# Kernel tuning notes

Measured on AMD Instinct MI355X. Metric: run time of the kernel, lower is better.

The kernel has to match this reference:

```python
import jax, jax.numpy as jnp
import numpy as np

B, S, D, H, FF, L, U = 64, 256, 128, 8, 512, 4, 5000
N, E, FEA, HW, CED, TD = 40000, 160000, 32, 16, 16, 6
DH = D // H


def _ln(x, g, b):
    m = jnp.mean(x, -1, keepdims=True)
    v = jnp.var(x, -1, keepdims=True)
    return (x - m) * jax.lax.rsqrt(v + 1e-5) * g + b


def _sin_pe(s, d):
    pos = jnp.arange(s, dtype=jnp.float32)[:, None]
    div = jnp.exp(jnp.arange(0, d, 2, dtype=jnp.float32) * (-np.log(10000.0) / d))
    ang = pos * div  # [S, D/2]
    return jnp.stack([jnp.sin(ang), jnp.cos(ang)], -1).reshape(s, d)


def setup_inputs() -> dict:
    key = jax.random.key(0)
    ks = jax.random.split(key, 40)
    sc = 0.02
    inp = {}
    inp['node_feature'] = jax.random.normal(ks[0], (N, FEA), jnp.float32)
    inp['edge_index'] = jax.random.randint(ks[1], (2, E), 0, N)
    inp['traj_x'] = jax.random.randint(ks[2], (B, S), 0, N)
    inp['temporal_x'] = jax.random.normal(ks[3], (B, S, TD), jnp.float32)
    inp['user_id_x'] = jax.random.randint(ks[4], (B, 1), 0, U)
    inp['mask'] = jnp.ones((B, S), jnp.int32)
    inp['end_idx'] = jax.random.randint(ks[5], (B,), 0, S)
    inp['idx_without_end'] = jax.random.randint(ks[6], (B,), 0, S)
    inp['temporal_mat_x'] = jax.random.uniform(ks[7], (B, S, S), jnp.float32) * 3600.0
    inp['dis_mat_x'] = jax.random.uniform(ks[8], (B, S, S), jnp.float32) * 5000.0
    inp['highway_x'] = jax.random.randint(ks[9], (B, S), 0, HW)
    inp['lambda2'] = jnp.float32(0.5)
    # --- learned parameters ---
    inp['gnn_w1'] = jax.random.normal(ks[10], (FEA, D), jnp.float32) * sc
    inp['gnn_b1'] = jnp.zeros((D,), jnp.float32)
    inp['gnn_w2'] = jax.random.normal(ks[11], (D, D), jnp.float32) * sc
    inp['gnn_b2'] = jnp.zeros((D,), jnp.float32)
    inp['ue_tab'] = jax.random.normal(ks[12], (U, D), jnp.float32) * sc
    inp['ce_tab'] = jax.random.normal(ks[13], (HW, CED), jnp.float32) * sc
    inp['fl_w'] = jax.random.normal(ks[14], (TD + CED, D), jnp.float32) * sc
    inp['fl_b'] = jnp.zeros((D,), jnp.float32)
    inp['wqkv'] = jax.random.normal(ks[15], (L, D, 3 * D), jnp.float32) * sc
    inp['bqkv'] = jnp.zeros((L, 3 * D), jnp.float32)
    inp['wo'] = jax.random.normal(ks[16], (L, D, D), jnp.float32) * sc
    inp['bo'] = jnp.zeros((L, D), jnp.float32)
    inp['ln1_g'] = jnp.ones((L, D), jnp.float32)
    inp['ln1_b'] = jnp.zeros((L, D), jnp.float32)
    inp['ln2_g'] = jnp.ones((L, D), jnp.float32)
    inp['ln2_b'] = jnp.zeros((L, D), jnp.float32)
    inp['ffn_w1'] = jax.random.normal(ks[17], (L, D, FF), jnp.float32) * sc
    inp['ffn_b1'] = jnp.zeros((L, FF), jnp.float32)
    inp['ffn_w2'] = jax.random.normal(ks[18], (L, FF, D), jnp.float32) * sc
    inp['ffn_b2'] = jnp.zeros((L, D), jnp.float32)
    inp['head_w'] = jax.random.normal(ks[19], (D, U), jnp.float32) * sc
    inp['head_b'] = jnp.zeros((U,), jnp.float32)
    return inp


def reference(node_feature, edge_index, traj_x, temporal_x, user_id_x, mask,
              end_idx, idx_without_end, temporal_mat_x, dis_mat_x, highway_x,
              lambda2,
              gnn_w1, gnn_b1, gnn_w2, gnn_b2, ue_tab, ce_tab, fl_w, fl_b,
              wqkv, bqkv, wo, bo, ln1_g, ln1_b, ln2_g, ln2_b,
              ffn_w1, ffn_b1, ffn_w2, ffn_b2, head_w, head_b):
    # --- spatial (road-network) GNN encoder: spe ---
    src, dst = edge_index[0], edge_index[1]
    deg = jax.ops.segment_sum(jnp.ones((E,), jnp.float32), dst, num_segments=N)
    h = node_feature
    for W, b in ((gnn_w1, gnn_b1), (gnn_w2, gnn_b2)):
        agg = jax.ops.segment_sum(h[src], dst, num_segments=N) / (deg[:, None] + 1.0)
        h = jax.nn.relu((h + agg) @ W + b)
    spe = h  # [N, D]
    # --- embedding fusion ---
    ce = ce_tab[highway_x]                                  # [B,S,CED]
    ue = ue_tab[user_id_x]                                  # [B,1,D] broadcast
    fuse = jax.nn.relu(jnp.concatenate([temporal_x, ce], -1) @ fl_w + fl_b)
    x = spe[traj_x] + ue + fuse                             # [B,S,D]
    x = x + _sin_pe(S, D)[None]
    # --- relative temporal/distance attention bias ---
    rel = lambda2 * jnp.log1p(temporal_mat_x) + (1.0 - lambda2) * jnp.log1p(dis_mat_x)
    mbias = jnp.where(mask[:, None, None, :] > 0, 0.0, -1e9)
    bias = mbias - rel[:, None]                             # [B,1,S,S]
    scale = 1.0 / float(np.sqrt(DH))
    for l in range(L):
        qkv = x @ wqkv[l] + bqkv[l]
        q, k, v = jnp.split(qkv, 3, axis=-1)
        q = q.reshape(B, S, H, DH).transpose(0, 2, 1, 3)
        k = k.reshape(B, S, H, DH).transpose(0, 2, 1, 3)
        v = v.reshape(B, S, H, DH).transpose(0, 2, 1, 3)
        scores = jnp.einsum('bhqd,bhkd->bhqk', q, k) * scale + bias
        a = jax.nn.softmax(scores, -1)
        o = jnp.einsum('bhqk,bhkd->bhqd', a, v).transpose(0, 2, 1, 3).reshape(B, S, D)
        x = _ln(x + o @ wo[l] + bo[l], ln1_g[l], ln1_b[l])
        f = jax.nn.relu(x @ ffn_w1[l] + ffn_b1[l]) @ ffn_w2[l] + ffn_b2[l]
        x = _ln(x + f, ln2_g[l], ln2_b[l])
    # --- gather last token + classifier head ---
    traj_emb = x[jnp.arange(B), end_idx]                    # [B,D]
    return traj_emb @ head_w + head_b                       # [B,U]
```

## Files before the change

### kernel.cpp

```cpp
#include <hip/hip_runtime.h>
#include <hip/hip_fp16.h>
#include <cstdint>
#include <cstddef>

typedef unsigned short u16;
typedef __attribute__((ext_vector_type(8))) short short8;
typedef __attribute__((ext_vector_type(4))) float f32x4;

#define B_   64
#define S_   256
#define D_   128
#define H_   8
#define DH_  16
#define FF_  512
#define L_   4
#define U_   5000
#define UP_  5120
#define N_   40000
#define NP_  40064
#define E_   160000
#define FEA_ 32
#define HWY_ 16
#define CED_ 16
#define TD_  6
#define NSCB 157
#define UB_CNT_END 160
#define UB_CVT_END 1592
#define UB_TOTAL   5688

static __device__ __forceinline__ u16 f2b(float f) {
    unsigned int u = __float_as_uint(f);
    unsigned int r = (u + 0x7FFFu + ((u >> 16) & 1u)) >> 16;
    return (u16)r;
}
static __device__ __forceinline__ float b2f(u16 u) {
    return __uint_as_float(((unsigned int)u) << 16);
}
static __device__ __forceinline__ u16 f2h(float f) {
    return __half_as_ushort(__float2half(f));
}
static __device__ __forceinline__ float h2f(u16 u) {
    return __half2float(__ushort_as_half(u));
}

static __device__ __forceinline__ void gload16(const void* g, void* l) {
    __builtin_amdgcn_global_load_lds(
        (const __attribute__((address_space(1))) unsigned int*)g,
        (__attribute__((address_space(3))) unsigned int*)l,
        16, 0, 0);
}

struct UberArgs {
    const float* csrc[7];
    u16* cdst[7];
    int K[7], Npad[7], Nsrc[7], Kp[7], base[7];
    const float* tm; const float* dm; const int* maskp; const float* lambda2;
    u16* bias; int* cnt;
};

__global__ __launch_bounds__(256) void k_uber(UberArgs a) {
    __shared__ float tile[32][33];
    int bid = blockIdx.x, tid = threadIdx.x;
    if (bid < UB_CNT_END) {
        int idx = bid * 256 + tid;
        if (idx < NP_) a.cnt[idx] = 0;
        return;
    }
    if (bid < UB_CVT_END) {
        int t = 0;
#pragma unroll
        for (int i = 1; i < 7; ++i) t += (bid >= a.base[i]);
        int rb = bid - a.base[t];
        int K = a.K[t], Npad = a.Npad[t], Nsrc = a.Nsrc[t], Kp = a.Kp[t];
        int nbn = Npad >> 5, nbk = Kp >> 5;
        int per = nbn * nbk;
        int l = rb / per, rem = rb - l * per;
        int n0 = (rem % nbn) * 32, k0 = (rem / nbn) * 32;
        const float* in = a.csrc[t];
        u16* outp = a.cdst[t];
        int j = tid & 31, i2 = tid >> 5;
#pragma unroll
        for (int r = 0; r < 4; ++r) {
            int k = k0 + i2 + r * 8, n = n0 + j;
            tile[i2 + r * 8][j] = (k < K && n < Nsrc) ? in[(size_t)l * K * Nsrc + (size_t)k * Nsrc + n] : 0.f;
        }
        __syncthreads();
#pragma unroll
        for (int r = 0; r < 4; ++r) {
            int n = n0 + i2 + r * 8, k = k0 + j;
            if (n < Npad && k < Kp)
                outp[(size_t)l * Npad * Kp + (size_t)n * Kp + k] = f2b(tile[j][i2 + r * 8]);
        }
        return;
    }
    int t4 = (bid - UB_CVT_END) * 256 + tid;
    const int total = B_ * S_ * S_ / 4;
    if (t4 >= total) return;
// ... 19 lines not shown
__global__ __launch_bounds__(256) void k_scanA(const int* __restrict__ cnt, int* __restrict__ part) {
    __shared__ int sh[256];
    int idx = blockIdx.x * 256 + threadIdx.x;
    sh[threadIdx.x] = (idx < NP_) ? cnt[idx] : 0;
    __syncthreads();
    for (int o = 128; o > 0; o >>= 1) {
        if (threadIdx.x < o) sh[threadIdx.x] += sh[threadIdx.x + o];
        __syncthreads();
    }
    if (threadIdx.x == 0) part[blockIdx.x] = sh[0];
}

__global__ __launch_bounds__(256) void k_scanB(const int* __restrict__ cnt, const int* __restrict__ part,
                                               int* __restrict__ off, int* __restrict__ cursor) {
    __shared__ int sh[256];
    __shared__ int bsum;
    int tid = threadIdx.x;
    int pv = (tid < blockIdx.x) ? part[tid] : 0;
    sh[tid] = pv;
    __syncthreads();
    for (int o = 128; o > 0; o >>= 1) {
        if (tid < o) sh[tid] += sh[tid + o];
        __syncthreads();
    }
    if (tid == 0) bsum = sh[0];
    __syncthreads();
    int basev = bsum;
    __syncthreads();
    int idx = blockIdx.x * 256 + tid;
    int v = (idx < NP_) ? cnt[idx] : 0;
    sh[tid] = v;
    __syncthreads();
    for (int o = 1; o < 256; o <<= 1) {
        int t2 = (tid >= o) ? sh[tid - o] : 0;
        __syncthreads();
        sh[tid] += t2;
        __syncthreads();
    }
    if (idx < NP_) {
        int res = sh[tid] - v + basev;
        off[idx] = res;
        cursor[idx] = res;
    }
}

__global__ __launch_bounds__(256) void k_fill(const int* __restrict__ src, const int* __restrict__ dst,
                                              int* __restrict__ cursor, int* __restrict__ ebuf) {
    int e = blockIdx.x * 256 + threadIdx.x;
    if (e >= E_) return;
    int p = atomicAdd(&cursor[dst[e]], 1);
    ebuf[p] = src[e];
}

__global__ __launch_bounds__(256) void k_gprep1(const float* __restrict__ nf, const int* __restrict__ off,
                                                const int* __restrict__ cnt, const int* __restrict__ ebuf,
                                                u16* __restrict__ out) {
    int n = blockIdx.x * 8 + (threadIdx.x >> 5);
    int f = threadIdx.x & 31;
    u16 r = 0;
    if (n < N_) {
        int start = off[n], c = cnt[n];
        float acc = 0.f;
        int i = 0;
        for (; i + 4 <= c; i += 4) {
            int s0 = ebuf[start + i], s1 = ebuf[start + i + 1];
            int s2 = ebuf[start + i + 2], s3 = ebuf[start + i + 3];
            float v0 = nf[(size_t)s0 * FEA_ + f];
            float v1 = nf[(size_t)s1 * FEA_ + f];
            float v2 = nf[(size_t)s2 * FEA_ + f];
            float v3 = nf[(size_t)s3 * FEA_ + f];
            acc += (v0 + v1) + (v2 + v3);
        }
        for (; i < c; ++i) {
            int s = ebuf[start + i];
            acc += nf[(size_t)s * FEA_ + f];
        }
        r = f2b(nf[(size_t)n * FEA_ + f] + acc / (float)(c + 1));
    }
    if (n < NP_) {
        out[(size_t)n * 64 + f] = r;
        out[(size_t)n * 64 + 32 + f] = 0;
    }
}

__global__ __launch_bounds__(256) void k_gprep2(const u16* __restrict__ h1b, const int* __restrict__ off,
                                                const int* __restrict__ cnt, const int* __restrict__ ebuf,
                                                u16* __restrict__ out) {
    int n = blockIdx.x * 4 + (threadIdx.x >> 6);
    int d2 = (threadIdx.x & 63) * 2;
    if (n >= NP_) return;
    u16 r0 = 0, r1 = 0;
    if (n < N_) {
        int start = off[n], c = cnt[n];
        float a0 = 0.f, a1 = 0.f;
        int i = 0;
        for (; i + 4 <= c; i += 4) {
            int s0 = ebuf[start + i], s1 = ebuf[start + i + 1];
            int s2 = ebuf[start + i + 2], s3 = ebuf[start + i + 3];
            ushort2 v0 = *(const ushort2*)&h1b[(size_t)s0 * D_ + d2];
            ushort2 v1 = *(const ushort2*)&h1b[(size_t)s1 * D_ + d2];
            ushort2 v2 = *(const ushort2*)&h1b[(size_t)s2 * D_ + d2];
            ushort2 v3 = *(const ushort2*)&h1b[(size_t)s3 * D_ + d2];
            a0 += (b2f(v0.x) + b2f(v1.x)) + (b2f(v2.x) + b2f(v3.x));
            a1 += (b2f(v0.y) + b2f(v1.y)) + (b2f(v2.y) + b2f(v3.y));
        }
        for (; i < c; ++i) {
            int s = ebuf[start + i];
            ushort2 v = *(const ushort2*)&h1b[(size_t)s * D_ + d2];
            a0 += b2f(v.x); a1 += b2f(v.y);
        }
        float rinv = 1.f / (float)(c + 1);
        ushort2 sv = *(const ushort2*)&h1b[(size_t)n * D_ + d2];
        r0 = f2b(b2f(sv.x) + a0 * rinv);
        r1 = f2b(b2f(sv.y) + a1 * rinv);
    }
    *(ushort2*)&out[(size_t)n * D_ + d2] = make_ushort2(r0, r1);
}

template<int BM, int ACT, int OUTB, int GAT>
__global__ __launch_bounds__(256) void k_mgemm(const u16* __restrict__ A, const u16* __restrict__ BT,
                                               const float* __restrict__ bias, void* __restrict__ Cout,
                                               const int* __restrict__ endi, int M, int N, int K) {
    constexpr int SMEMB = (BM == 128) ? 32768 : 24576;
    __shared__ __align__(16) char smem[SMEMB];
    u16* Al = (u16*)smem;
    u16* Bl = Al + (BM == 128 ? 128 * 64 : 64 * 64);
    int tid = threadIdx.x;
    int wid = tid >> 6, lane = tid & 63;
    int row0 = blockIdx.x * BM;
    int col0 = blockIdx.y * 128;
    f32x4 acc[4][4] = {};
    int rA = lane & 15, kq = lane >> 4;

    for (int k0 = 0; k0 < K; k0 += 64) {
        if (k0) __syncthreads();
        if (BM == 128) {
            int srow = wid * 32 + (lane >> 3);
            int ks8 = ((lane & 7) ^ (lane >> 3)) * 8;
#pragma unroll
            for (int i = 0; i < 4; ++i) {
                int row = srow + i * 8;
                size_t arow = (size_t)(row0 + row);
                if (GAT) {
                    int bb2 = row0 + row;
                    arow = (bb2 < B_) ? ((size_t)bb2 * S_ + endi[bb2]) : 0;
                }
                gload16(A + arow * K + k0 + ks8, &Al[(wid * 32 + i * 8) * 64]);
                gload16(BT + (size_t)(col0 + row) * K + k0 + ks8, &Bl[(wid * 32 + i * 8) * 64]);
            }
        } else {
#pragma unroll
            for (int i = 0; i < 6; ++i) {
                int c = wid * 6 + i;
                int rr = c * 8 + (lane >> 3);
                int sl = (((lane & 7) ^ (rr & 7)) << 3);
                if (c < 8) {
                    size_t arow = (size_t)(row0 + rr);
                    if (GAT) {
                        int bb2 = row0 + rr;
                        arow = (bb2 < B_) ? ((size_t)bb2 * S_ + endi[bb2]) : 0;
                    }
                    gload16(A + arow * K + k0 + sl, &Al[rr * 64]);
                } else {
                    gload16(BT + (size_t)(col0 + rr - 64) * K + k0 + sl, &Bl[(rr - 64) * 64]);
                }
            }
        }
        __syncthreads();
#pragma unroll
        for (int ks = 0; ks < 2; ++ks) {
            int sw = ((ks * 4 + kq) ^ (rA & 7)) * 8;
            if (BM == 128) {
                int wr = wid >> 1, wc = wid & 1;
                short8 af[4], bfr[4];
#pragma unroll
                for (int m = 0; m < 4; ++m)
                    af[m] = *(const short8*)&Al[(64 * wr + m * 16 + rA) * 64 + sw];
#pragma unroll
                for (int n = 0; n < 4; ++n)
                    bfr[n] = *(const short8*)&Bl[(64 * wc + n * 16 + rA) * 64 + sw];
#pragma unroll
                for (int m = 0; m < 4; ++m)
#pragma unroll
                    for (int n = 0; n < 4; ++n)
                        acc[m][n] = __builtin_amdgcn_mfma_f32_16x16x32_bf16(af[m], bfr[n], acc[m][n], 0, 0, 0);
            } else {
                int wr2 = wid & 1, wc2 = wid >> 1;
                short8 af[2], bfr[4];
#pragma unroll
                for (int m = 0; m < 2; ++m)
                    af[m] = *(const short8*)&Al[(wr2 * 32 + m * 16 + rA) * 64 + sw];
#pragma unroll
                for (int n = 0; n < 4; ++n)
                    bfr[n] = *(const short8*)&Bl[(wc2 * 64 + n * 16 + rA) * 64 + sw];
#pragma unroll
                for (int m = 0; m < 2; ++m)
#pragma unroll
                    for (int n = 0; n < 4; ++n)
                        acc[m][n] = __builtin_amdgcn_mfma_f32_16x16x32_bf16(af[m], bfr[n], acc[m][n], 0, 0, 0);
            }
        }
    }

    constexpr int MR = (BM == 128) ? 4 : 2;
#pragma unroll
    for (int m = 0; m < MR; ++m) {
#pragma unroll
        for (int n = 0; n < 4; ++n) {
            int cc, cr0;
            if (BM == 128) { cc = col0 + (wid & 1) * 64 + n * 16 + rA; cr0 = row0 + (wid >> 1) * 64 + m * 16 + kq * 4; }
            else           { cc = col0 + (wid >> 1) * 64 + n * 16 + rA; cr0 = row0 + (wid & 1) * 32 + m * 16 + kq * 4; }
            if (cc >= N) continue;
            float bv = bias[cc];
#pragma unroll
            for (int r = 0; r < 4; ++r) {
                int cr = cr0 + r;
                if (cr >= M) continue;
                float v = acc[m][n][r] + bv;
                if (ACT) v = fmaxf(v, 0.f);
                if (OUTB) ((u16*)Cout)[(size_t)cr * N + cc] = f2b(v);
                else      ((float*)Cout)[(size_t)cr * N + cc] = v;
            }
        }
    }
}

#define KLS 40
#define VTS 272
__global__ __launch_bounds__(256) void k_qkvatt(const u16* __restrict__ xb, const u16* __restrict__ wT,
                                                const float* __restrict__ bq, const u16* __restrict__ bias,
                                                u16* __restrict__ o) {
    __shared__ __align__(16) char smem[73728];
    u16* Kl  = (u16*)smem;
    u16* Vt  = (u16*)(smem + 20480);
    u16* Ql  = (u16*)(smem + 29184);
    u16* Pl  = (u16*)(smem + 37376);
    u16* Ast = (u16*)smem;
    u16* Bst = (u16*)(smem + 32768);
    int idx = blockIdx.x;
    int b = (idx & 7) * 8 + (idx >> 6);
    int h = (idx >> 3) & 7;
    int tid = threadIdx.x, wid = tid >> 6, lane = tid & 63;
    int rA = lane & 15, kq = lane >> 4;

    f32x4 acc[4][3] = {};
    for (int k0 = 0; k0 < 128; k0 += 64) {
        if (k0) __syncthreads();
#pragma unroll
        for (int i = 0; i < 8; ++i) {
            int row = wid * 64 + i * 8 + (lane >> 3);
            int sl = (((lane & 7) ^ (row & 7)) << 3);
            gload16(xb + ((size_t)(b * S_ + row)) * 128 + k0 + sl, &Ast[(wid * 64 + i * 8) * 64]);
        }
        if (wid < 3) {
#pragma unroll
            for (int i = 0; i < 2; ++i) {
                int c = wid * 2 + i;
                int brow = c * 8 + (lane >> 3);
                int grow = wid * 128 + h * 16 + (brow & 15);
                int sl = (((lane & 7) ^ (brow & 7)) << 3);
                gload16(wT + (size_t)grow * 128 + k0 + sl, &Bst[c * 8 * 64]);
            }
        }
        __syncthreads();
#pragma unroll
        for (int ks = 0; ks < 2; ++ks) {
            int sw = ((ks * 4 + kq) ^ (rA & 7)) * 8;
            short8 af[4], bfr[3];
#pragma unroll
            for (int m = 0; m < 4; ++m)
                af[m] = *(const short8*)&Ast[(wid * 64 + m * 16 + rA) * 64 + sw];
#pragma unroll
            for (int n = 0; n < 3; ++n)
                bfr[n] = *(const short8*)&Bst[(n * 16 + rA) * 64 + sw];
#pragma unroll
            for (int m = 0; m < 4; ++m)
#pragma unroll
                for (int n = 0; n < 3; ++n)
                    acc[m][n] = __builtin_amdgcn_mfma_f32_16x16x32_bf16(af[m], bfr[n], acc[m][n], 0, 0, 0);
        }
    }
    __syncthreads();
    {
        short8 z = {};
        *(short8*)&Kl[tid * KLS + 16] = z;
        *(short8*)&Kl[tid * KLS + 24] = z;
    }
    {
        float bq0 = bq[h * 16 + rA];
        float bq1 = bq[128 + h * 16 + rA];
        float bq2 = bq[256 + h * 16 + rA];
#pragma unroll
        for (int m = 0; m < 4; ++m) {
            int cr0 = wid * 64 + m * 16 + kq * 4;
#pragma unroll
            for (int r = 0; r < 4; ++r) {
                int row = cr0 + r;
                Ql[row * 16 + rA]  = f2b(acc[m][0][r] + bq0);
                Kl[row * KLS + rA] = f2b(acc[m][1][r] + bq1);
                Vt[rA * VTS + row] = f2b(acc[m][2][r] + bq2);
            }
        }
    }
    __syncthreads();

    u16* pl = Pl + wid * 16 * VTS;
    int qi = lane & 15;
    for (int qt = 0; qt < 4; ++qt) {
        int q = wid * 64 + qt * 16 + qi;
        ushort4 bb[16];
        const u16* bp = bias + (size_t)b * (S_ * S_) + (size_t)q * S_ + kq * 4;
#pragma unroll
        for (int t = 0; t < 16; ++t) bb[t] = *(const ushort4*)(bp + t * 16);
        short8 qf = {};
        if (lane < 32)
            qf = *(const short8*)&Ql[q * 16 + kq * 8];
        f32x4 sc[16];
#pragma unroll
        for (int t = 0; t < 16; ++t) {
            short8 kf = *(const short8*)&Kl[(t * 16 + qi) * KLS + kq * 8];
            f32x4 zz = {0.f, 0.f, 0.f, 0.f};
            sc[t] = __builtin_amdgcn_mfma_f32_16x16x32_bf16(kf, qf, zz, 0, 0, 0);
        }
        float m = -1e30f;
#pragma unroll
        for (int t = 0; t < 16; ++t) {
            sc[t][0] = sc[t][0] * 0.25f + h2f(bb[t].x);
            sc[t][1] = sc[t][1] * 0.25f + h2f(bb[t].y);
            sc[t][2] = sc[t][2] * 0.25f + h2f(bb[t].z);
            sc[t][3] = sc[t][3] * 0.25f + h2f(bb[t].w);
            m = fmaxf(m, fmaxf(fmaxf(sc[t][0], sc[t][1]), fmaxf(sc[t][2], sc[t][3])));
        }
        m = fmaxf(m, __shfl_xor(m, 16, 64));
        m = fmaxf(m, __shfl_xor(m, 32, 64));
        float l = 0.f;
#pragma unroll
        for (int t = 0; t < 16; ++t) {
            sc[t][0] = __expf(sc[t][0] - m);
            sc[t][1] = __expf(sc[t][1] - m);
            sc[t][2] = __expf(sc[t][2] - m);
            sc[t][3] = __expf(sc[t][3] - m);
            l += (sc[t][0] + sc[t][1]) + (sc[t][2] + sc[t][3]);
        }
        l += __shfl_xor(l, 16, 64);
        l += __shfl_xor(l, 32, 64);
        float inv = 1.f / l;
#pragma unroll
        for (int t = 0; t < 16; ++t) {
            ushort4 pw = make_ushort4(f2b(sc[t][0] * inv), f2b(sc[t][1] * inv),
                                      f2b(sc[t][2] * inv), f2b(sc[t][3] * inv));
            *(ushort4*)&pl[qi * VTS + t * 16 + kq * 4] = pw;
        }
        f32x4 oa = {0.f, 0.f, 0.f, 0.f};
#pragma unroll
        for (int w8 = 0; w8 < 8; ++w8) {
            short8 vf = *(const short8*)&Vt[qi * VTS + w8 * 32 + kq * 8];
            short8 pf = *(const short8*)&pl[qi * VTS + w8 * 32 + kq * 8];
            oa = __builtin_amdgcn_mfma_f32_16x16x32_bf16(vf, pf, oa, 0, 0, 0);
        }
        ushort4 ow = make_ushort4(f2b(oa[0]), f2b(oa[1]), f2b(oa[2]), f2b(oa[3]));
        *(ushort4*)&o[((size_t)(b * S_ + q)) * D_ + h * 16 + kq * 4] = ow;
    }
}

__global__ __launch_bounds__(256) void k_layer(const u16* __restrict__ atto,
                                               const u16* __restrict__ woT, const float* __restrict__ bo,
                                               const float* __restrict__ ln1g, const float* __restrict__ ln1b,
                                               const u16* __restrict__ w1T, const float* __restrict__ b1,
                                               const u16* __restrict__ w2T, const float* __restrict__ b2,
                                               const float* __restrict__ ln2g, const float* __restrict__ ln2b,
                                               float* __restrict__ x, u16* __restrict__ xbout) {
    __shared__ __align__(16) char smem[73728];
    u16* Alds = (u16*)smem;
    u16* Wlds = (u16*)(smem + 8192);
    u16* f1   = (u16*)(smem + 40960);
    float* vbuf = (float*)smem;
    int tid = threadIdx.x, wid = tid >> 6, lane = tid & 63;
    int rows0 = blockIdx.x * 32;
    int rA = lane & 15, kq = lane >> 4;
    int row = tid >> 3, sub = tid & 7;

#pragma unroll
    for (int j = 0; j < 2; ++j) {
        int srow = wid * 8 + j * 4 + (lane >> 4);
        int win = (lane >> 3) & 1, slot = lane & 7;
        gload16(atto + (size_t)(rows0 + srow) * 128 + win * 64 + ((slot ^ (srow & 7)) << 3),
                Alds + (wid * 8 + j * 4) * 128);
    }

    f32x4 accw[2][2] = {};
    for (int k0 = 0; k0 < 128; k0 += 64) {
        __syncthreads();
#pragma unroll
        for (int i = 0; i < 4; ++i) {
            int rl2 = i * 32 + wid * 8 + (lane >> 3);
            gload16(woT + (size_t)rl2 * 128 + k0 + (((lane & 7) ^ (rl2 & 7)) << 3),
                    Wlds + (i * 32 + wid * 8) * 64);
        }
        __syncthreads();
#pragma unroll
        for (int ks = 0; ks < 2; ++ks) {
            int sw = ((ks * 4 + kq) ^ (rA & 7)) << 3;
            short8 af0 = *(const short8*)&Alds[rA * 128 + k0 + sw];
            short8 af1 = *(const short8*)&Alds[(16 + rA) * 128 + k0 + sw];
            short8 bf0 = *(const short8*)&Wlds[(wid * 32 + rA) * 64 + sw];
            short8 bf1 = *(const short8*)&Wlds[(wid * 32 + 16 + rA) * 64 + sw];
            accw[0][0] = __builtin_amdgcn_mfma_f32_16x16x32_bf16(af0, bf0, accw[0][0], 0, 0, 0);
            accw[0][1] = __builtin_amdgcn_mfma_f32_16x16x32_bf16(af0, bf1, accw[0][1], 0, 0, 0);
            accw[1][0] = __builtin_amdgcn_mfma_f32_16x16x32_bf16(af1, bf0, accw[1][0], 0, 0, 0);
            accw[1][1] = __builtin_amdgcn_mfma_f32_16x16x32_bf16(af1, bf1, accw[1][1], 0, 0, 0);
        }
    }

    __syncthreads();
#pragma unroll
    for (int m = 0; m < 2; ++m)
#pragma unroll
        for (int n = 0; n < 2; ++n) {
            int cc = wid * 32 + n * 16 + rA;
            float bv = bo[cc];
#pragma unroll
            for (int r = 0; r < 4; ++r) {
                int rl = m * 16 + kq * 4 + r;
                vbuf[rl * 133 + cc] = accw[m][n][r] + bv + x[(size_t)(rows0 + rl) * 128 + cc];
            }
        }
    __syncthreads();
    float x1[16];
    {
        const float* vr = vbuf + row * 133 + sub * 16;
        float s = 0.f, s2 = 0.f;
#pragma unroll
        for (int j = 0; j < 16; ++j) {
            x1[j] = vr[j];
            s += x1[j];
            s2 += x1[j] * x1[j];
        }
        s += __shfl_xor(s, 1, 64);  s2 += __shfl_xor(s2, 1, 64);
        s += __shfl_xor(s, 2, 64);  s2 += __shfl_xor(s2, 2, 64);
        s += __shfl_xor(s, 4, 64);  s2 += __shfl_xor(s2, 4, 64);
        float mean = s * (1.f / 128.f);
        float var = s2 * (1.f / 128.f) - mean * mean;
        float rs = rsqrtf(var + 1e-5f);
#pragma unroll
        for (int j = 0; j < 4; ++j) {
            float4 gv = *(const float4*)(ln1g + sub * 16 + j * 4);
            float4 bv = *(const float4*)(ln1b + sub * 16 + j * 4);
            x1[j * 4 + 0] = (x1[j * 4 + 0] - mean) * rs * gv.x + bv.x;
            x1[j * 4 + 1] = (x1[j * 4 + 1] - mean) * rs * gv.y + bv.y;
            x1[j * 4 + 2] = (x1[j * 4 + 2] - mean) * rs * gv.z + bv.z;
            x1[j * 4 + 3] = (x1[j * 4 + 3] - mean) * rs * gv.w + bv.w;
        }
    }
    __syncthreads();
#pragma unroll
    for (int j = 0; j < 16; ++j) {
        int c = sub * 16 + j;
        int sc = (c & ~63) | ((((c >> 3) & 7) ^ (row & 7)) << 3) | (c & 7);
        Alds[row * 128 + sc] = f2b(x1[j]);
    }

    for (int nh = 0; nh < 2; ++nh) {
        f32x4 acc1[2][4] = {};
        for (int k0 = 0; k0 < 128; k0 += 64) {
            __syncthreads();
#pragma unroll
            for (int i = 0; i < 8; ++i) {
                int rl2 = i * 32 + wid * 8 + (lane >> 3);
                gload16(w1T + (size_t)(nh * 256 + rl2) * 128 + k0 + (((lane & 7) ^ (rl2 & 7)) << 3),
                        Wlds + (i * 32 + wid * 8) * 64);
            }
            __syncthreads();
#pragma unroll
            for (int ks = 0; ks < 2; ++ks) {
                int sw = ((ks * 4 + kq) ^ (rA & 7)) << 3;
                short8 af[2], bf4[4];
                af[0] = *(const short8*)&Alds[rA * 128 + k0 + sw];
                af[1] = *(const short8*)&Alds[(16 + rA) * 128 + k0 + sw];
#pragma unroll
                for (int n = 0; n < 4; ++n)
                    bf4[n] = *(const short8*)&Wlds[(wid * 64 + n * 16 + rA) * 64 + sw];
#pragma unroll
                for (int m = 0; m < 2; ++m)
#pragma unroll
                    for (int n = 0; n < 4; ++n)
                        acc1[m][n] = __builtin_amdgcn_mfma_f32_16x16x32_bf16(af[m], bf4[n], acc1[m][n], 0, 0, 0);
            }
        }
#pragma unroll
        for (int m = 0; m < 2; ++m)
#pragma unroll
            for (int n = 0; n < 4; ++n) {
                int cc = nh * 256 + wid * 64 + n * 16 + rA;
                float bv = b1[cc];
#pragma unroll
                for (int r = 0; r < 4; ++r) {
                    int rl = m * 16 + kq * 4 + r;
                    float v = fmaxf(acc1[m][n][r] + bv, 0.f);
                    int scol = (cc & ~63) | (((((cc >> 3) & 7) ^ (rl & 7)) & 7) << 3) | (cc & 7);
                    f1[rl * 512 + scol] = f2b(v);
                }
            }
    }
    __syncthreads();

    f32x4 acc2[2][2] = {};
    for (int k0 = 0; k0 < 512; k0 += 64) {
        if (k0) __syncthreads();
#pragma unroll
        for (int i = 0; i < 4; ++i) {
            int rl2 = i * 32 + wid * 8 + (lane >> 3);
            gload16(w2T + (size_t)rl2 * 512 + k0 + (((lane & 7) ^ (rl2 & 7)) << 3),
                    Wlds + (i * 32 + wid * 8) * 64);
        }
        __syncthreads();
#pragma unroll
        for (int ks = 0; ks < 2; ++ks) {
            int sw = ((ks * 4 + kq) ^ (rA & 7)) << 3;
            short8 af0 = *(const short8*)&f1[rA * 512 + k0 + sw];
            short8 af1 = *(const short8*)&f1[(16 + rA) * 512 + k0 + sw];
            short8 bf0 = *(const short8*)&Wlds[(wid * 32 + rA) * 64 + sw];
            short8 bf1 = *(const short8*)&Wlds[(wid * 32 + 16 + rA) * 64 + sw];
            acc2[0][0] = __builtin_amdgcn_mfma_f32_16x16x32_bf16(af0, bf0, acc2[0][0], 0, 0, 0);
            acc2[0][1] = __builtin_amdgcn_mfma_f32_16x16x32_bf16(af0, bf1, acc2[0][1], 0, 0, 0);
            acc2[1][0] = __builtin_amdgcn_mfma_f32_16x16x32_bf16(af1, bf0, acc2[1][0], 0, 0, 0);
            acc2[1][1] = __builtin_amdgcn_mfma_f32_16x16x32_bf16(af1, bf1, acc2[1][1], 0, 0, 0);
        }
    }

    __syncthreads();
#pragma unroll
    for (int m = 0; m < 2; ++m)
#pragma unroll
        for (int n = 0; n < 2; ++n) {
            int cc = wid * 32 + n * 16 + rA;
            float bv = b2[cc];
#pragma unroll
            for (int r = 0; r < 4; ++r) {
                int rl = m * 16 + kq * 4 + r;
                vbuf[rl * 133 + cc] = acc2[m][n][r] + bv;
            }
        }
    __syncthreads();
    {
        const float* vr = vbuf + row * 133 + sub * 16;
        float vv[16];
        float s = 0.f, s2 = 0.f;
#pragma unroll
        for (int j = 0; j < 16; ++j) {
            vv[j] = vr[j] + x1[j];
            s += vv[j];
            s2 += vv[j] * vv[j];
        }
        s += __shfl_xor(s, 1, 64);  s2 += __shfl_xor(s2, 1, 64);
        s += __shfl_xor(s, 2, 64);  s2 += __shfl_xor(s2, 2, 64);
        s += __shfl_xor(s, 4, 64);  s2 += __shfl_xor(s2, 4, 64);
        float mean = s * (1.f / 128.f);
        float var = s2 * (1.f / 128.f) - mean * mean;
        float rs = rsqrtf(var + 1e-5f);
        int grow = rows0 + row;
        float* xrow = x + (size_t)grow * 128 + sub * 16;
        u16* xbrow = xbout + (size_t)grow * 128 + sub * 16;
#pragma unroll
        for (int j = 0; j < 4; ++j) {
            float4 gv = *(const float4*)(ln2g + sub * 16 + j * 4);
            float4 bv = *(const float4*)(ln2b + sub * 16 + j * 4);
            float o0 = (vv[j * 4 + 0] - mean) * rs * gv.x + bv.x;
            float o1 = (vv[j * 4 + 1] - mean) * rs * gv.y + bv.y;
            float o2 = (vv[j * 4 + 2] - mean) * rs * gv.z + bv.z;
            float o3 = (vv[j * 4 + 3] - mean) * rs * gv.w + bv.w;
            *(float4*)(xrow + j * 4) = make_float4(o0, o1, o2, o3);
            *(ushort4*)(xbrow + j * 4) = make_ushort4(f2b(o0), f2b(o1), f2b(o2), f2b(o3));
        }
    }
}

__global__ __launch_bounds__(256) void k_fusion(const float* __restrict__ spe, const int* __restrict__ traj,
                                                const float* __restrict__ ue_tab, const int* __restrict__ uid,
                                                const float* __restrict__ tempx, const int* __restrict__ hwx,
                                                const float* __restrict__ ce_tab, const float* __restrict__ flw,
                                                const float* __restrict__ flb, float* __restrict__ x,
                                                u16* __restrict__ xb) {
// ... 28 lines not shown

extern "C" void kernel_launch(void* const* d_in, const int* in_sizes, int n_in,
                              void* d_out, int out_size, void* d_ws, size_t ws_size,
                              hipStream_t stream) {
    const float* node_feature = (const float*)d_in[0];
    const int*   edge_index   = (const int*)d_in[1];
    const int*   traj_x       = (const int*)d_in[2];
    const float* temporal_x   = (const float*)d_in[3];
    const int*   user_id_x    = (const int*)d_in[4];
    const int*   mask         = (const int*)d_in[5];
    const int*   end_idx      = (const int*)d_in[6];
    const float* tmat         = (const float*)d_in[8];
    const float* dmat         = (const float*)d_in[9];
    const int*   highway_x    = (const int*)d_in[10];
    const float* lambda2      = (const float*)d_in[11];
    const float* gnn_w1       = (const float*)d_in[12];
    const float* gnn_b1       = (const float*)d_in[13];
    const float* gnn_w2       = (const float*)d_in[14];
    const float* gnn_b2       = (const float*)d_in[15];
    const float* ue_tab       = (const float*)d_in[16];
    const float* ce_tab       = (const float*)d_in[17];
    const float* fl_w         = (const float*)d_in[18];
    const float* fl_b         = (const float*)d_in[19];
    const float* wqkv         = (const float*)d_in[20];
    const float* bqkv         = (const float*)d_in[21];
    const float* wo           = (const float*)d_in[22];
    const float* bo           = (const float*)d_in[23];
    const float* ln1_g        = (const float*)d_in[24];
    const float* ln1_b        = (const float*)d_in[25];
    const float* ln2_g        = (const float*)d_in[26];
    const float* ln2_b        = (const float*)d_in[27];
    const float* ffn_w1       = (const float*)d_in[28];
    const float* ffn_b1       = (const float*)d_in[29];
    const float* ffn_w2       = (const float*)d_in[30];
    const float* ffn_b2       = (const float*)d_in[31];
    const float* head_w       = (const float*)d_in[32];
    const float* head_b       = (const float*)d_in[33];
    float* out = (float*)d_out;

    float* w     = (float*)d_ws;
    int*   cnt   = (int*)w;
    float* spe   = w + 40960;
    u16*   biasb = (u16*)(w + 5169152);
    float* wreg  = w + 7266304;
    u16* wqkvT = (u16*)wreg;
    u16* woT   = wqkvT + 4 * 384 * 128;
    u16* w1T   = woT + 4 * 128 * 128;
    u16* w2T   = w1T + 4 * 512 * 128;
    u16* gw1T  = w2T + 4 * 128 * 512;
    u16* gw2T  = gw1T + 128 * 64;
    u16* hwT   = gw2T + 128 * 128;
    float* pool  = w + 8000000;
    u16*   h1b   = (u16*)pool;
    u16*   in1b  = (u16*)(pool + 2564096);
    u16*   in2b  = (u16*)(pool + 3846144);
    int*   off   = (int*)(pool + 6410240);
    int*   cursor= (int*)(pool + 6450304);
    int*   ebuf  = (int*)(pool + 6490368);
    int*   part  = (int*)(pool + 6650368);
    float* x     = pool;
    u16*   xb    = (u16*)(pool + 2097152);
    u16*   attob = (u16*)(pool + 4718592);

    const int* esrc = edge_index;
    const int* edst = edge_index + E_;

    UberArgs ua;
    const float* srcs[7] = {wqkv, wo, ffn_w1, ffn_w2, gnn_w1, gnn_w2, head_w};
    u16* dsts[7]        = {wqkvT, woT, w1T, w2T, gw1T, gw2T, hwT};
    int Ks[7]    = {128, 128, 128, 512, 32, 128, 128};
    int Npads[7] = {384, 128, 512, 128, 128, 128, UP_};
    int Nsrcs[7] = {384, 128, 512, 128, 128, 128, U_};
    int Kps[7]   = {128, 128, 128, 512, 64, 128, 128};
    int Ls[7]    = {4, 4, 4, 4, 1, 1, 1};
    int bb = UB_CNT_END;
    for (int t = 0; t < 7; ++t) {
        ua.csrc[t] = srcs[t]; ua.cdst[t] = dsts[t];
        ua.K[t] = Ks[t]; ua.Npad[t] = Npads[t]; ua.Nsrc[t] = Nsrcs[t]; ua.Kp[t] = Kps[t];
        ua.base[t] = bb;
        bb += (Npads[t] / 32) * (Kps[t] / 32) * Ls[t];
    }
    ua.tm = tmat; ua.dm = dmat; ua.maskp = mask; ua.lambda2 = lambda2;
    ua.bias = biasb; ua.cnt = cnt;
    k_uber<<<UB_TOTAL, 256, 0, stream>>>(ua);

    k_count<<<(E_ + 255) / 256, 256, 0, stream>>>(edst, cnt);
    k_scanA<<<NSCB, 256, 0, stream>>>(cnt, part);
    k_scanB<<<NSCB, 256, 0, stream>>>(cnt, part, off, cursor);
    k_fill<<<(E_ + 255) / 256, 256, 0, stream>>>(esrc, edst, cursor, ebuf);
    k_gprep1<<<NP_ / 8, 256, 0, stream>>>(node_feature, off, cnt, ebuf, in1b);
    k_mgemm<128, 1, 1, 0><<<dim3(NP_ / 128, 1), 256, 0, stream>>>(in1b, gw1T, gnn_b1, h1b, nullptr, NP_, D_, 64);
    k_gprep2<<<NP_ / 4, 256, 0, stream>>>(h1b, off, cnt, ebuf, in2b);
    k_mgemm<128, 1, 0, 0><<<dim3(NP_ / 128, 1), 256, 0, stream>>>(in2b, gw2T, gnn_b2, spe, nullptr, NP_, D_, D_);

    k_fusion<<<(B_ * S_) / 32, 256, 0, stream>>>(spe, traj_x, ue_tab, user_id_x,
                                                 temporal_x, highway_x, ce_tab, fl_w, fl_b, x, xb);

    const int M = B_ * S_;
    for (int l = 0; l < L_; ++l) {
        k_qkvatt<<<B_ * H_, 256, 0, stream>>>(xb, wqkvT + (size_t)l * 384 * 128,
                                              bqkv + (size_t)l * 384, biasb, attob);
        k_layer<<<M / 32, 256, 0, stream>>>(attob, woT + (size_t)l * 128 * 128, bo + l * D_,
                                            ln1_g + l * D_, ln1_b + l * D_,
                                            w1T + (size_t)l * 512 * 128, ffn_b1 + l * FF_,
                                            w2T + (size_t)l * 128 * 512, ffn_b2 + l * D_,
                                            ln2_g + l * D_, ln2_b + l * D_, x, xb);
    }

    k_mgemm<64, 0, 0, 1><<<dim3(1, UP_ / 128), 256, 0, stream>>>(xb, hwT, head_b, out, end_idx, B_, U_, D_);
}
```

Measured before the change: 303.2 us.

## Fuse GNN neighbor aggregation into the GEMM kernels, skipping intermediate buffers

The GNN mean-aggregation prep kernels are merged into their following MFMA GEMMs. Each block gathers and averages the neighbor features for its 128 rows straight into swizzled LDS and then runs the GEMM on that tile. This removes two kernel launches and the global round trip of the in1b and in2b intermediates. The head GEMM is specialised into its own kernel and workspace offsets are repacked. The cost is that the gather phase now runs inside GEMM blocks with a larger LDS footprint, which may lower occupancy during the latency-bound gathers.

After: 350.7 us. +15.7%, slower.

```diff
diff --git a/kernel.cpp b/kernel.cpp
--- a/kernel.cpp
+++ b/kernel.cpp
@@ -11,7 +11,6 @@
 #define S_   256
 #define D_   128
 #define H_   8
-#define DH_  16
 #define FF_  512
 #define L_   4
 #define U_   5000
@@ -20,13 +19,14 @@
 #define NP_  40064
 #define E_   160000
 #define FEA_ 32
-#define HWY_ 16
 #define CED_ 16
 #define TD_  6
 #define NSCB 157
 #define UB_CNT_END 160
 #define UB_CVT_END 1592
 #define UB_TOTAL   5688
+#define KLS 40
+#define VTS 272
 
 static __device__ __forceinline__ u16 f2b(float f) {
     unsigned int u = __float_as_uint(f);
@@ -42,7 +42,6 @@
 static __device__ __forceinline__ float h2f(u16 u) {
     return __half2float(__ushort_as_half(u));
 }
-
 static __device__ __forceinline__ void gload16(const void* g, void* l) {
     __builtin_amdgcn_global_load_lds(
         (const __attribute__((address_space(1))) unsigned int*)g,
@@ -168,181 +167,224 @@
     ebuf[p] = src[e];
 }
 
-__global__ __launch_bounds__(256) void k_gprep1(const float* __restrict__ nf, const int* __restrict__ off,
+__global__ __launch_bounds__(256) void k_ggemm1(const float* __restrict__ nf, const int* __restrict__ off,
                                                 const int* __restrict__ cnt, const int* __restrict__ ebuf,
-                                                u16* __restrict__ out) {
-    int n = blockIdx.x * 8 + (threadIdx.x >> 5);
-    int f = threadIdx.x & 31;
-    u16 r = 0;
-    if (n < N_) {
-        int start = off[n], c = cnt[n];
-        float acc = 0.f;
-        int i = 0;
-        for (; i + 4 <= c; i += 4) {
-            int s0 = ebuf[start + i], s1 = ebuf[start + i + 1];
-            int s2 = ebuf[start + i + 2], s3 = ebuf[start + i + 3];
-            float v0 = nf[(size_t)s0 * FEA_ + f];
-            float v1 = nf[(size_t)s1 * FEA_ + f];
-            float v2 = nf[(size_t)s2 * FEA_ + f];
-            float v3 = nf[(size_t)s3 * FEA_ + f];
-            acc += (v0 + v1) + (v2 + v3);
-        }
-        for (; i < c; ++i) {
-            int s = ebuf[start + i];
-            acc += nf[(size_t)s * FEA_ + f];
-        }
-        r = f2b(nf[(size_t)n * FEA_ + f] + acc / (float)(c + 1));
-    }
-    if (n < NP_) {
-        out[(size_t)n * 64 + f] = r;
-        out[(size_t)n * 64 + 32 + f] = 0;
-    }
-}
-
-__global__ __launch_bounds__(256) void k_gprep2(const u16* __restrict__ h1b, const int* __restrict__ off,
+                                                const u16* __restrict__ gw1T, const float* __restrict__ b1,
+                                                u16* __restrict__ h1b) {
+    __shared__ u16 Al[128 * 64];
+    __shared__ u16 Bl[128 * 64];
+    int tid = threadIdx.x, wid = tid >> 6, lane = tid & 63;
+    int rows0 = blockIdx.x * 128;
+#pragma unroll
+    for (int i = 0; i < 4; ++i) {
+        int rr = wid * 32 + i * 8 + (lane >> 3);
+        gload16(gw1T + (size_t)rr * 64 + (((lane & 7) ^ (rr & 7)) << 3), &Bl[(wid * 32 + i * 8) * 64]);
+    }
+    int f = tid & 31;
+    int c = f >> 3, fo = f & 7;
+    for (int it = 0; it < 16; ++it) {
+        int rl = it * 8 + (tid >> 5);
+        int n = rows0 + rl;
+        u16 r = 0;
+        if (n < N_) {
+            int start = off[n], cdeg = cnt[n];
+            float acc = 0.f;
+            int i = 0;
+            for (; i + 4 <= cdeg; i += 4) {
+                int s0 = ebuf[start + i], s1 = ebuf[start + i + 1];
+                int s2 = ebuf[start + i + 2], s3 = ebuf[start + i + 3];
+                float v0 = nf[(size_t)s0 * FEA_ + f];
+                float v1 = nf[(size_t)s1 * FEA_ + f];
+                float v2 = nf[(size_t)s2 * FEA_ + f];
+                float v3 = nf[(size_t)s3 * FEA_ + f];
+                acc += (v0 + v1) + (v2 + v3);
+            }
+            for (; i < cdeg; ++i) acc += nf[(size_t)ebuf[start + i] * FEA_ + f];
+            r = f2b(nf[(size_t)n * FEA_ + f] + acc / (float)(cdeg + 1));
+        }
+        Al[rl * 64 + ((c ^ (rl & 7)) << 3) + fo] = r;
+        Al[rl * 64 + (((c + 4) ^ (rl & 7)) << 3) + fo] = 0;
+    }
+    __syncthreads();
+    int rA = lane & 15, kq = lane >> 4;
+    int wr = wid >> 1, wc = wid & 1;
+    f32x4 acc[4][4] = {};
+#pragma unroll
+    for (int ks = 0; ks < 2; ++ks) {
+        int sw = ((ks * 4 + kq) ^ (rA & 7)) * 8;
+        short8 af[4], bfr[4];
+#pragma unroll
+        for (int m = 0; m < 4; ++m)
+            af[m] = *(const short8*)&Al[(64 * wr + m * 16 + rA) * 64 + sw];
+#pragma unroll
+        for (int n = 0; n < 4; ++n)
+            bfr[n] = *(const short8*)&Bl[(64 * wc + n * 16 + rA) * 64 + sw];
+#pragma unroll
+        for (int m = 0; m < 4; ++m)
+#pragma unroll
+            for (int n = 0; n < 4; ++n)
+                acc[m][n] = __builtin_amdgcn_mfma_f32_16x16x32_bf16(af[m], bfr[n], acc[m][n], 0, 0, 0);
+    }
+#pragma unroll
+    for (int m = 0; m < 4; ++m)
+#pragma unroll
+        for (int n = 0; n < 4; ++n) {
+            int cc = (wid & 1) * 64 + n * 16 + rA;
+            float bv = b1[cc];
+#pragma unroll
+            for (int r = 0; r < 4; ++r) {
+                int cr = rows0 + (wid >> 1) * 64 + m * 16 + kq * 4 + r;
+                h1b[(size_t)cr * 128 + cc] = f2b(fmaxf(acc[m][n][r] + bv, 0.f));
+            }
+        }
+}
+
+__global__ __launch_bounds__(256) void k_ggemm2(const u16* __restrict__ h1b, const int* __restrict__ off,
                                                 const int* __restrict__ cnt, const int* __restrict__ ebuf,
-                                                u16* __restrict__ out) {
-    int n = blockIdx.x * 4 + (threadIdx.x >> 6);
-    int d2 = (threadIdx.x & 63) * 2;
-    if (n >= NP_) return;
-    u16 r0 = 0, r1 = 0;
-    if (n < N_) {
-        int start = off[n], c = cnt[n];
-        float a0 = 0.f, a1 = 0.f;
-        int i = 0;
-        for (; i + 4 <= c; i += 4) {
-            int s0 = ebuf[start + i], s1 = ebuf[start + i + 1];
-            int s2 = ebuf[start + i + 2], s3 = ebuf[start + i + 3];
-            ushort2 v0 = *(const ushort2*)&h1b[(size_t)s0 * D_ + d2];
-            ushort2 v1 = *(const ushort2*)&h1b[(size_t)s1 * D_ + d2];
-            ushort2 v2 = *(const ushort2*)&h1b[(size_t)s2 * D_ + d2];
-            ushort2 v3 = *(const ushort2*)&h1b[(size_t)s3 * D_ + d2];
-            a0 += (b2f(v0.x) + b2f(v1.x)) + (b2f(v2.x) + b2f(v3.x));
-            a1 += (b2f(v0.y) + b2f(v1.y)) + (b2f(v2.y) + b2f(v3.y));
-        }
-        for (; i < c; ++i) {
-            int s = ebuf[start + i];
-            ushort2 v = *(const ushort2*)&h1b[(size_t)s * D_ + d2];
-            a0 += b2f(v.x); a1 += b2f(v.y);
-        }
-        float rinv = 1.f / (float)(c + 1);
-        ushort2 sv = *(const ushort2*)&h1b[(size_t)n * D_ + d2];
-        r0 = f2b(b2f(sv.x) + a0 * rinv);
-        r1 = f2b(b2f(sv.y) + a1 * rinv);
-    }
-    *(ushort2*)&out[(size_t)n * D_ + d2] = make_ushort2(r0, r1);
-}
-
-template<int BM, int ACT, int OUTB, int GAT>
-__global__ __launch_bounds__(256) void k_mgemm(const u16* __restrict__ A, const u16* __restrict__ BT,
-                                               const float* __restrict__ bias, void* __restrict__ Cout,
-                                               const int* __restrict__ endi, int M, int N, int K) {
-    constexpr int SMEMB = (BM == 128) ? 32768 : 24576;
-    __shared__ __align__(16) char smem[SMEMB];
+                                                const u16* __restrict__ gw2T, const float* __restrict__ b2,
+                                                float* __restrict__ spe) {
+    __shared__ u16 Al[128 * 128];
+    __shared__ u16 Bl[128 * 64];
+    int tid = threadIdx.x, wid = tid >> 6, lane = tid & 63;
+    int rows0 = blockIdx.x * 128;
+    int d2 = (tid & 63) * 2;
+    int w = d2 >> 6, cch = (d2 >> 3) & 7, fo = d2 & 7;
+    for (int it = 0; it < 32; ++it) {
+        int rl = it * 4 + (tid >> 6);
+        int n = rows0 + rl;
+        u16 r0 = 0, r1 = 0;
+        if (n < N_) {
+            int start = off[n], cdeg = cnt[n];
+            float a0 = 0.f, a1 = 0.f;
+            int i = 0;
+            for (; i + 4 <= cdeg; i += 4) {
+                int s0 = ebuf[start + i], s1 = ebuf[start + i + 1];
+                int s2 = ebuf[start + i + 2], s3 = ebuf[start + i + 3];
+                ushort2 v0 = *(const ushort2*)&h1b[(size_t)s0 * D_ + d2];
+                ushort2 v1 = *(const ushort2*)&h1b[(size_t)s1 * D_ + d2];
+                ushort2 v2 = *(const ushort2*)&h1b[(size_t)s2 * D_ + d2];
+                ushort2 v3 = *(const ushort2*)&h1b[(size_t)s3 * D_ + d2];
+                a0 += (b2f(v0.x) + b2f(v1.x)) + (b2f(v2.x) + b2f(v3.x));
+                a1 += (b2f(v0.y) + b2f(v1.y)) + (b2f(v2.y) + b2f(v3.y));
+            }
+            for (; i < cdeg; ++i) {
+                ushort2 v = *(const ushort2*)&h1b[(size_t)ebuf[start + i] * D_ + d2];
+                a0 += b2f(v.x); a1 += b2f(v.y);
+            }
+            float rinv = 1.f / (float)(cdeg + 1);
+            ushort2 sv = *(const ushort2*)&h1b[(size_t)n * D_ + d2];
+            r0 = f2b(b2f(sv.x) + a0 * rinv);
+            r1 = f2b(b2f(sv.y) + a1 * rinv);
+        }
+        int pos = rl * 128 + w * 64 + ((cch ^ (rl & 7)) << 3) + fo;
+        Al[pos] = r0;
+        Al[pos + 1] = r1;
+    }
+    int rA = lane & 15, kq = lane >> 4;
+    int wr = wid >> 1, wc = wid & 1;
+    f32x4 acc[4][4] = {};
+    for (int k0 = 0; k0 < 128; k0 += 64) {
+        if (k0) __syncthreads();
+#pragma unroll
+        for (int i = 0; i < 4; ++i) {
+            int rr = wid * 32 + i * 8 + (lane >> 3);
+            gload16(gw2T + (size_t)rr * 128 + k0 + (((lane & 7) ^ (rr & 7)) << 3), &Bl[(wid * 32 + i * 8) * 64]);
+        }
+        __syncthreads();
+#pragma unroll
+        for (int ks = 0; ks < 2; ++ks) {
+            int sw = ((ks * 4 + kq) ^ (rA & 7)) * 8;
+            short8 af[4], bfr[4];
+#pragma unroll
+            for (int m = 0; m < 4; ++m)
+                af[m] = *(const short8*)&Al[(64 * wr + m * 16 + rA) * 128 + k0 + sw];
+#pragma unroll
+            for (int n = 0; n < 4; ++n)
+                bfr[n] = *(const short8*)&Bl[(64 * wc + n * 16 + rA) * 64 + sw];
+#pragma unroll
+            for (int m = 0; m < 4; ++m)
+#pragma unroll
+                for (int n = 0; n < 4; ++n)
+                    acc[m][n] = __builtin_amdgcn_mfma_f32_16x16x32_bf16(af[m], bfr[n], acc[m][n], 0, 0, 0);
+        }
+    }
+#pragma unroll
+    for (int m = 0; m < 4; ++m)
+#pragma unroll
+        for (int n = 0; n < 4; ++n) {
+            int cc = (wid & 1) * 64 + n * 16 + rA;
+            float bv = b2[cc];
+#pragma unroll
+            for (int r = 0; r < 4; ++r) {
+                int cr = rows0 + (wid >> 1) * 64 + m * 16 + kq * 4 + r;
+                spe[(size_t)cr * 128 + cc] = fmaxf(acc[m][n][r] + bv, 0.f);
+            }
+        }
+}
+
+__global__ __launch_bounds__(256) void k_head(const u16* __restrict__ A, const u16* __restrict__ BT,
+                                              const float* __restrict__ bias, float* __restrict__ Cout,
+                                              const int* __restrict__ endi, int M, int N, int K) {
+    __shared__ __align__(16) char smem[24576];
     u16* Al = (u16*)smem;
-    u16* Bl = Al + (BM == 128 ? 128 * 64 : 64 * 64);
+    u16* Bl = Al + 64 * 64;
     int tid = threadIdx.x;
     int wid = tid >> 6, lane = tid & 63;
-    int row0 = blockIdx.x * BM;
     int col0 = blockIdx.y * 128;
-    f32x4 acc[4][4] = {};
+    f32x4 acc[2][4] = {};
     int rA = lane & 15, kq = lane >> 4;
 
     for (int k0 = 0; k0 < K; k0 += 64) {
         if (k0) __syncthreads();
-        if (BM == 128) {
-            int srow = wid * 32 + (lane >> 3);
-            int ks8 = ((lane & 7) ^ (lane >> 3)) * 8;
-#pragma unroll
-            for (int i = 0; i < 4; ++i) {
-                int row = srow + i * 8;
-                size_t arow = (size_t)(row0 + row);
-                if (GAT) {
-                    int bb2 = row0 + row;
-                    arow = (bb2 < B_) ? ((size_t)bb2 * S_ + endi[bb2]) : 0;
-                }
-                gload16(A + arow * K + k0 + ks8, &Al[(wid * 32 + i * 8) * 64]);
-                gload16(BT + (size_t)(col0 + row) * K + k0 + ks8, &Bl[(wid * 32 + i * 8) * 64]);
-            }
-        } else {
-#pragma unroll
-            for (int i = 0; i < 6; ++i) {
-                int c = wid * 6 + i;
-                int rr = c * 8 + (lane >> 3);
-                int sl = (((lane & 7) ^ (rr & 7)) << 3);
-                if (c < 8) {
-                    size_t arow = (size_t)(row0 + rr);
-                    if (GAT) {
-                        int bb2 = row0 + rr;
-                        arow = (bb2 < B_) ? ((size_t)bb2 * S_ + endi[bb2]) : 0;
-                    }
-                    gload16(A + arow * K + k0 + sl, &Al[rr * 64]);
-                } else {
-                    gload16(BT + (size_t)(col0 + rr - 64) * K + k0 + sl, &Bl[(rr - 64) * 64]);
-                }
+#pragma unroll
+        for (int i = 0; i < 6; ++i) {
+            int c = wid * 6 + i;
+            int rr = c * 8 + (lane >> 3);
+            int sl = (((lane & 7) ^ (rr & 7)) << 3);
+            if (c < 8) {
+                size_t arow = (rr < B_) ? ((size_t)rr * S_ + endi[rr]) : 0;
+                gload16(A + arow * K + k0 + sl, &Al[rr * 64]);
+            } else {
+                gload16(BT + (size_t)(col0 + rr - 64) * K + k0 + sl, &Bl[(rr - 64) * 64]);
             }
         }
         __syncthreads();
 #pragma unroll
         for (int ks = 0; ks < 2; ++ks) {
             int sw = ((ks * 4 + kq) ^ (rA & 7)) * 8;
-            if (BM == 128) {
-                int wr = wid >> 1, wc = wid & 1;
-                short8 af[4], bfr[4];
-#pragma unroll
-                for (int m = 0; m < 4; ++m)
-                    af[m] = *(const short8*)&Al[(64 * wr + m * 16 + rA) * 64 + sw];
+            int wr2 = wid & 1, wc2 = wid >> 1;
+            short8 af[2], bfr[4];
+#pragma unroll
+            for (int m = 0; m < 2; ++m)
+                af[m] = *(const short8*)&Al[(wr2 * 32 + m * 16 + rA) * 64 + sw];
+#pragma unroll
+            for (int n = 0; n < 4; ++n)
+                bfr[n] = *(const short8*)&Bl[(wc2 * 64 + n * 16 + rA) * 64 + sw];
+#pragma unroll
+            for (int m = 0; m < 2; ++m)
 #pragma unroll
                 for (int n = 0; n < 4; ++n)
-                    bfr[n] = *(const short8*)&Bl[(64 * wc + n * 16 + rA) * 64 + sw];
-#pragma unroll
-                for (int m = 0; m < 4; ++m)
-#pragma unroll
-                    for (int n = 0; n < 4; ++n)
-                        acc[m][n] = __builtin_amdgcn_mfma_f32_16x16x32_bf16(af[m], bfr[n], acc[m][n], 0, 0, 0);
-            } else {
-                int wr2 = wid & 1, wc2 = wid >> 1;
-                short8 af[2], bfr[4];
-#pragma unroll
-                for (int m = 0; m < 2; ++m)
-                    af[m] = *(const short8*)&Al[(wr2 * 32 + m * 16 + rA) * 64 + sw];
-#pragma unroll
-                for (int n = 0; n < 4; ++n)
-                    bfr[n] = *(const short8*)&Bl[(wc2 * 64 + n * 16 + rA) * 64 + sw];
-#pragma unroll
-                for (int m = 0; m < 2; ++m)
-#pragma unroll
-                    for (int n = 0; n < 4; ++n)
-                        acc[m][n] = __builtin_amdgcn_mfma_f32_16x16x32_bf16(af[m], bfr[n], acc[m][n], 0, 0, 0);
-            }
-        }
-    }
-
-    constexpr int MR = (BM == 128) ? 4 : 2;
-#pragma unroll
-    for (int m = 0; m < MR; ++m) {
+                    acc[m][n] = __builtin_amdgcn_mfma_f32_16x16x32_bf16(af[m], bfr[n], acc[m][n], 0, 0, 0);
+        }
+    }
+#pragma unroll
+    for (int m = 0; m < 2; ++m) {
 #pragma unroll
         for (int n = 0; n < 4; ++n) {
-            int cc, cr0;
-            if (BM == 128) { cc = col0 + (wid & 1) * 64 + n * 16 + rA; cr0 = row0 + (wid >> 1) * 64 + m * 16 + kq * 4; }
-            else           { cc = col0 + (wid >> 1) * 64 + n * 16 + rA; cr0 = row0 + (wid & 1) * 32 + m * 16 + kq * 4; }
+            int cc = col0 + (wid >> 1) * 64 + n * 16 + rA;
+            int cr0 = (wid & 1) * 32 + m * 16 + kq * 4;
             if (cc >= N) continue;
             float bv = bias[cc];
 #pragma unroll
             for (int r = 0; r < 4; ++r) {
                 int cr = cr0 + r;
                 if (cr >= M) continue;
-                float v = acc[m][n][r] + bv;
-                if (ACT) v = fmaxf(v, 0.f);
-                if (OUTB) ((u16*)Cout)[(size_t)cr * N + cc] = f2b(v);
-                else      ((float*)Cout)[(size_t)cr * N + cc] = v;
-            }
-        }
-    }
-}
-
-#define KLS 40
-#define VTS 272
+                Cout[(size_t)cr * N + cc] = acc[m][n][r] + bv;
+            }
+        }
+    }
+}
+
 __global__ __launch_bounds__(256) void k_qkvatt(const u16* __restrict__ xb, const u16* __restrict__ wT,
                                                 const float* __restrict__ bq, const u16* __restrict__ bias,
                                                 u16* __restrict__ o) {
@@ -449,18 +491,18 @@
         }
         m = fmaxf(m, __shfl_xor(m, 16, 64));
         m = fmaxf(m, __shfl_xor(m, 32, 64));
-        float l = 0.f;
+        float lsum = 0.f;
 #pragma unroll
         for (int t = 0; t < 16; ++t) {
             sc[t][0] = __expf(sc[t][0] - m);
             sc[t][1] = __expf(sc[t][1] - m);
             sc[t][2] = __expf(sc[t][2] - m);
             sc[t][3] = __expf(sc[t][3] - m);
-            l += (sc[t][0] + sc[t][1]) + (sc[t][2] + sc[t][3]);
-        }
-        l += __shfl_xor(l, 16, 64);
-        l += __shfl_xor(l, 32, 64);
-        float inv = 1.f / l;
+            lsum += (sc[t][0] + sc[t][1]) + (sc[t][2] + sc[t][3]);
+        }
+        lsum += __shfl_xor(lsum, 16, 64);
+        lsum += __shfl_xor(lsum, 32, 64);
+        float inv = 1.f / lsum;
 #pragma unroll
         for (int t = 0; t < 16; ++t) {
             ushort4 pw = make_ushort4(f2b(sc[t][0] * inv), f2b(sc[t][1] * inv),
@@ -503,7 +545,6 @@
         gload16(atto + (size_t)(rows0 + srow) * 128 + win * 64 + ((slot ^ (srow & 7)) << 3),
                 Alds + (wid * 8 + j * 4) * 128);
     }
-
     f32x4 accw[2][2] = {};
     for (int k0 = 0; k0 < 128; k0 += 64) {
         __syncthreads();
@@ -527,7 +568,6 @@
             accw[1][1] = __builtin_amdgcn_mfma_f32_16x16x32_bf16(af1, bf1, accw[1][1], 0, 0, 0);
         }
     }
-
     __syncthreads();
 #pragma unroll
     for (int m = 0; m < 2; ++m)
@@ -572,10 +612,9 @@
 #pragma unroll
     for (int j = 0; j < 16; ++j) {
         int c = sub * 16 + j;
-        int sc = (c & ~63) | ((((c >> 3) & 7) ^ (row & 7)) << 3) | (c & 7);
-        Alds[row * 128 + sc] = f2b(x1[j]);
-    }
-
+        int scol = (c & ~63) | ((((c >> 3) & 7) ^ (row & 7)) << 3) | (c & 7);
+        Alds[row * 128 + scol] = f2b(x1[j]);
+    }
     for (int nh = 0; nh < 2; ++nh) {
         f32x4 acc1[2][4] = {};
         for (int k0 = 0; k0 < 128; k0 += 64) {
@@ -619,7 +658,6 @@
             }
     }
     __syncthreads();
-
     f32x4 acc2[2][2] = {};
     for (int k0 = 0; k0 < 512; k0 += 64) {
         if (k0) __syncthreads();
@@ -643,7 +681,6 @@
             acc2[1][1] = __builtin_amdgcn_mfma_f32_16x16x32_bf16(af1, bf1, acc2[1][1], 0, 0, 0);
         }
     }
-
     __syncthreads();
 #pragma unroll
     for (int m = 0; m < 2; ++m)
@@ -778,14 +815,12 @@
     u16* hwT   = gw2T + 128 * 128;
     float* pool  = w + 8000000;
     u16*   h1b   = (u16*)pool;
-    u16*   in1b  = (u16*)(pool + 2564096);
-    u16*   in2b  = (u16*)(pool + 3846144);
-    int*   off   = (int*)(pool + 6410240);
-    int*   cursor= (int*)(pool + 6450304);
-    int*   ebuf  = (int*)(pool + 6490368);
-    int*   part  = (int*)(pool + 6650368);
+    int*   off   = (int*)(pool + 2564096);
+    int*   cursor= (int*)(pool + 2604160);
+    int*   ebuf  = (int*)(pool + 2644224);
+    int*   part  = (int*)(pool + 2804224);
     float* x     = pool;
-    u16*   xb    = (u16*)(pool + 2097152);
+    u16*   xb    = (u16*)(pool + 3145728);
     u16*   attob = (u16*)(pool + 4718592);
 
     const int* esrc = edge_index;
@@ -814,24 +849,21 @@
     k_scanA<<<NSCB, 256, 0, stream>>>(cnt, part);
     k_scanB<<<NSCB, 256, 0, stream>>>(cnt, part, off, cursor);
     k_fill<<<(E_ + 255) / 256, 256, 0, stream>>>(esrc, edst, cursor, ebuf);
-    k_gprep1<<<NP_ / 8, 256, 0, stream>>>(node_feature, off, cnt, ebuf, in1b);
-    k_mgemm<128, 1, 1, 0><<<dim3(NP_ / 128, 1), 256, 0, stream>>>(in1b, gw1T, gnn_b1, h1b, nullptr, NP_, D_, 64);
-    k_gprep2<<<NP_ / 4, 256, 0, stream>>>(h1b, off, cnt, ebuf, in2b);
-    k_mgemm<128, 1, 0, 0><<<dim3(NP_ / 128, 1), 256, 0, stream>>>(in2b, gw2T, gnn_b2, spe, nullptr, NP_, D_, D_);
+    k_ggemm1<<<NP_ / 128, 256, 0, stream>>>(node_feature, off, cnt, ebuf, gw1T, gnn_b1, h1b);
+    k_ggemm2<<<NP_ / 128, 256, 0, stream>>>(h1b, off, cnt, ebuf, gw2T, gnn_b2, spe);
 
     k_fusion<<<(B_ * S_) / 32, 256, 0, stream>>>(spe, traj_x, ue_tab, user_id_x,
                                                  temporal_x, highway_x, ce_tab, fl_w, fl_b, x, xb);
 
-    const int M = B_ * S_;
     for (int l = 0; l < L_; ++l) {
         k_qkvatt<<<B_ * H_, 256, 0, stream>>>(xb, wqkvT + (size_t)l * 384 * 128,
                                               bqkv + (size_t)l * 384, biasb, attob);
-        k_layer<<<M / 32, 256, 0, stream>>>(attob, woT + (size_t)l * 128 * 128, bo + l * D_,
-                                            ln1_g + l * D_, ln1_b + l * D_,
-                                            w1T + (size_t)l * 512 * 128, ffn_b1 + l * FF_,
-                                            w2T + (size_t)l * 128 * 512, ffn_b2 + l * D_,
-                                            ln2_g + l * D_, ln2_b + l * D_, x, xb);
-    }
-
-    k_mgemm<64, 0, 0, 1><<<dim3(1, UP_ / 128), 256, 0, stream>>>(xb, hwT, head_b, out, end_idx, B_, U_, D_);
-}
+        k_layer<<<(B_ * S_) / 32, 256, 0, stream>>>(attob, woT + (size_t)l * 128 * 128, bo + l * D_,
+                                                    ln1_g + l * D_, ln1_b + l * D_,
+                                                    w1T + (size_t)l * 512 * 128, ffn_b1 + l * FF_,
+                                                    w2T + (size_t)l * 128 * 512, ffn_b2 + l * D_,
+                                                    ln2_g + l * D_, ln2_b + l * D_, x, xb);
+    }
+
+    k_head<<<dim3(1, UP_ / 128), 256, 0, stream>>>(xb, hwT, head_b, out, end_idx, B_, U_, D_);
+}
```
